# Kernel tuning notes

Measured on AMD Instinct MI355X. Metric: run time of the kernel, lower is better.

## Reference

```python
import jax, jax.numpy as jnp
import numpy as np


def setup_inputs() -> dict:
    key = jax.random.key(0)
    k1, k2 = jax.random.split(key)
    pred = jax.random.normal(k1, (4, 4096, 3), dtype=jnp.float32)
    gt = jax.random.normal(k2, (4, 4096, 3), dtype=jnp.float32)
    return {"pred": pred, "gt": gt}


def reference(pred, gt):
    # Chamfer distance with L1 (Manhattan) point-to-point distance.
    # pred: [B, N, 3], gt: [B, M, 3]
    # d[b, n, m] = sum_c |pred[b,n,c] - gt[b,m,c]|
    d = jnp.abs(pred[:, :, None, :] - gt[:, None, :, :]).sum(-1)  # [B, N, M]
    cham_x = d.min(axis=2).mean(axis=1)  # nearest gt for each pred point, [B]
    cham_y = d.min(axis=1).mean(axis=1)  # nearest pred for each gt point, [B]
    # point_reduction='mean' per direction, batch_reduction='mean' (pytorch3d default)
    return jnp.mean(cham_x + cham_y)
```

## Files before the change

### kernel.cpp

```cpp
#include <hip/hip_runtime.h>
#include <cfloat>


constexpr int TPB = 256;
constexpr int PTS = 4;
constexpr int NC  = TPB * PTS;
constexpr int MC  = 256;

__global__ __launch_bounds__(TPB) void chamfer_partial_kernel(
    const float* __restrict__ pred, const float* __restrict__ gt,
    unsigned* __restrict__ wsmin, int B, int N, int M) {
    const int dir = blockIdx.z;
    const int b   = blockIdx.y;
    const float* q = dir ? gt   : pred;
    const float* t = dir ? pred : gt;
    const int Nq   = dir ? M : N;
    const int Nt   = dir ? N : M;
    const int nchunks = Nq / NC;
    const int nc = blockIdx.x % nchunks;
    const int mc = blockIdx.x / nchunks;

    __shared__ float4 lds4[MC];

    const float* tbase = t + ((size_t)b * Nt + (size_t)mc * MC) * 3;
    for (int i = threadIdx.x; i < MC * 3; i += TPB) {
        ((float*)&lds4[i / 3])[i % 3] = tbase[i];
    }
    __syncthreads();

    const float* qb = q + (size_t)b * Nq * 3;
    float px[PTS], py[PTS], pz[PTS], mn[PTS];
    int n[PTS];
#pragma unroll
    for (int i = 0; i < PTS; ++i) {
        n[i] = nc * NC + threadIdx.x + i * TPB;
        px[i] = qb[n[i] * 3 + 0];
        py[i] = qb[n[i] * 3 + 1];
        pz[i] = qb[n[i] * 3 + 2];
        mn[i] = FLT_MAX;
    }

#pragma unroll 4
    for (int j = 0; j < MC; j += 2) {
        float4 g0 = lds4[j];
        float4 g1 = lds4[j + 1];
#pragma unroll
        for (int i = 0; i < PTS; ++i) {
            float d0 = fabsf(px[i] - g0.x) + fabsf(py[i] - g0.y) + fabsf(pz[i] - g0.z);
            float d1 = fabsf(px[i] - g1.x) + fabsf(py[i] - g1.y) + fabsf(pz[i] - g1.z);
            mn[i] = fminf(mn[i], fminf(d0, d1));
        }
    }

    unsigned* outp = wsmin + ((size_t)dir * B + b) * N;
#pragma unroll
    for (int i = 0; i < PTS; ++i)
        atomicMin(&outp[n[i]], __float_as_uint(mn[i]));
}

__global__ __launch_bounds__(256) void chamfer_reduce_kernel(
    const unsigned* __restrict__ wsmin, float* __restrict__ out, float inv) {
    const int qidx = blockIdx.x * 256 + threadIdx.x;
    float v = __uint_as_float(wsmin[qidx]) * inv;

    for (int off = 32; off > 0; off >>= 1) v += __shfl_down(v, off, 64);
    __shared__ float red[4];
    const int lane = threadIdx.x & 63, w = threadIdx.x >> 6;
    if (lane == 0) red[w] = v;
    __syncthreads();
    if (threadIdx.x == 0)
        atomicAdd(out, red[0] + red[1] + red[2] + red[3]);
}

extern "C" void kernel_launch(void* const* d_in, const int* in_sizes, int n_in,
                              void* d_out, int out_size, void* d_ws, size_t ws_size,
                              hipStream_t stream) {
    const float* pred = (const float*)d_in[0];
    const float* gt   = (const float*)d_in[1];
    float* out = (float*)d_out;

    const int B = 4;
    const int N = in_sizes[0] / (B * 3);
    const int M = in_sizes[1] / (B * 3);

    unsigned* wsmin = (unsigned*)d_ws;
    const int nmc = M / MC;
    const int Q = 2 * B * N;

    hipMemsetAsync(out, 0, sizeof(float), stream);
    hipMemsetAsync(wsmin, 0xFF, (size_t)Q * sizeof(unsigned), stream);

    dim3 grid((N / NC) * nmc, B, 2);
    chamfer_partial_kernel<<<grid, TPB, 0, stream>>>(pred, gt, wsmin, B, N, M);

    chamfer_reduce_kernel<<<Q / 256, 256, 0, stream>>>(
        wsmin, out, 1.0f / (float)(B * N));
}
```

Measured before the change: 79.15 us.

## Fuse final reduction into partial kernel via last-block counter and SoA LDS

Merges the reduce kernel into the distance kernel: each block increments a global counter after its atomicMin writes, and the last block to arrive sums all per-point minima and writes the output directly. This removes one kernel launch and one memset. It also changes the shared-memory tile from float4-per-point to a structure-of-arrays layout, so each float4 read covers four target points per coordinate and the inner loop processes four points per step. The counter starts at 0xFFFFFFFF from the memset, which is why the last-block test compares against nblocks-2. The cost is a serial final sum over all minima inside a single block.

```diff
diff --git a/kernel.cpp b/kernel.cpp
--- a/kernel.cpp
+++ b/kernel.cpp
@@ -7,9 +7,11 @@
 constexpr int NC  = TPB * PTS;
 constexpr int MC  = 256;
 
-__global__ __launch_bounds__(TPB) void chamfer_partial_kernel(
+__global__ __launch_bounds__(TPB) void chamfer_fused_kernel(
     const float* __restrict__ pred, const float* __restrict__ gt,
-    unsigned* __restrict__ wsmin, int B, int N, int M) {
+    unsigned* __restrict__ wsmin, unsigned* __restrict__ counter,
+    float* __restrict__ out,
+    int B, int N, int M, int nblocks, float inv) {
     const int dir = blockIdx.z;
     const int b   = blockIdx.y;
     const float* q = dir ? gt   : pred;
@@ -20,11 +22,13 @@
     const int nc = blockIdx.x % nchunks;
     const int mc = blockIdx.x / nchunks;
 
-    __shared__ float4 lds4[MC];
+    __shared__ __align__(16) float lds[3 * MC];
+    __shared__ float red[4];
+    __shared__ int lastFlag;
 
     const float* tbase = t + ((size_t)b * Nt + (size_t)mc * MC) * 3;
     for (int i = threadIdx.x; i < MC * 3; i += TPB) {
-        ((float*)&lds4[i / 3])[i % 3] = tbase[i];
+        lds[(i % 3) * MC + i / 3] = tbase[i];
     }
     __syncthreads();
 
@@ -40,15 +44,19 @@
         mn[i] = FLT_MAX;
     }
 
-#pragma unroll 4
-    for (int j = 0; j < MC; j += 2) {
-        float4 g0 = lds4[j];
-        float4 g1 = lds4[j + 1];
+#pragma unroll 2
+    for (int j = 0; j < MC; j += 4) {
+        float4 gx = *(const float4*)&lds[j];
+        float4 gy = *(const float4*)&lds[MC + j];
+        float4 gz = *(const float4*)&lds[2 * MC + j];
 #pragma unroll
         for (int i = 0; i < PTS; ++i) {
-            float d0 = fabsf(px[i] - g0.x) + fabsf(py[i] - g0.y) + fabsf(pz[i] - g0.z);
-            float d1 = fabsf(px[i] - g1.x) + fabsf(py[i] - g1.y) + fabsf(pz[i] - g1.z);
+            float d0 = fabsf(px[i] - gx.x) + fabsf(py[i] - gy.x) + fabsf(pz[i] - gz.x);
+            float d1 = fabsf(px[i] - gx.y) + fabsf(py[i] - gy.y) + fabsf(pz[i] - gz.y);
+            float d2 = fabsf(px[i] - gx.z) + fabsf(py[i] - gy.z) + fabsf(pz[i] - gz.z);
+            float d3 = fabsf(px[i] - gx.w) + fabsf(py[i] - gy.w) + fabsf(pz[i] - gz.w);
             mn[i] = fminf(mn[i], fminf(d0, d1));
+            mn[i] = fminf(mn[i], fminf(d2, d3));
         }
     }
 
@@ -56,20 +64,33 @@
 #pragma unroll
     for (int i = 0; i < PTS; ++i)
         atomicMin(&outp[n[i]], __float_as_uint(mn[i]));
-}
 
-__global__ __launch_bounds__(256) void chamfer_reduce_kernel(
-    const unsigned* __restrict__ wsmin, float* __restrict__ out, float inv) {
-    const int qidx = blockIdx.x * 256 + threadIdx.x;
-    float v = __uint_as_float(wsmin[qidx]) * inv;
+    __threadfence();
+    if (threadIdx.x == 0) {
+        unsigned old = __hip_atomic_fetch_add(counter, 1u, __ATOMIC_ACQ_REL,
+                                              __HIP_MEMORY_SCOPE_AGENT);
+        lastFlag = (old == (unsigned)(nblocks - 2));
+    }
+    __syncthreads();
+    if (!lastFlag) return;
+    __threadfence();
+
+    const unsigned long long* w2 = (const unsigned long long*)wsmin;
+    const int total2 = B * N;
+    float v = 0.0f;
+    for (int i = threadIdx.x; i < total2; i += TPB) {
+        unsigned long long u = __hip_atomic_load(&w2[i], __ATOMIC_RELAXED,
+                                                 __HIP_MEMORY_SCOPE_AGENT);
+        v += __uint_as_float((unsigned)u) + __uint_as_float((unsigned)(u >> 32));
+    }
+    v *= inv;
 
     for (int off = 32; off > 0; off >>= 1) v += __shfl_down(v, off, 64);
-    __shared__ float red[4];
     const int lane = threadIdx.x & 63, w = threadIdx.x >> 6;
     if (lane == 0) red[w] = v;
     __syncthreads();
     if (threadIdx.x == 0)
-        atomicAdd(out, red[0] + red[1] + red[2] + red[3]);
+        *out = red[0] + red[1] + red[2] + red[3];
 }
 
 extern "C" void kernel_launch(void* const* d_in, const int* in_sizes, int n_in,
@@ -83,16 +104,15 @@
     const int N = in_sizes[0] / (B * 3);
     const int M = in_sizes[1] / (B * 3);
 
-    unsigned* wsmin = (unsigned*)d_ws;
-    const int nmc = M / MC;
+    unsigned* wsmin   = (unsigned*)d_ws;
     const int Q = 2 * B * N;
+    unsigned* counter = wsmin + Q;
 
-    hipMemsetAsync(out, 0, sizeof(float), stream);
-    hipMemsetAsync(wsmin, 0xFF, (size_t)Q * sizeof(unsigned), stream);
+    hipMemsetAsync(d_ws, 0xFF, (size_t)(Q + 16) * sizeof(unsigned), stream);
 
-    dim3 grid((N / NC) * nmc, B, 2);
-    chamfer_partial_kernel<<<grid, TPB, 0, stream>>>(pred, gt, wsmin, B, N, M);
-
-    chamfer_reduce_kernel<<<Q / 256, 256, 0, stream>>>(
-        wsmin, out, 1.0f / (float)(B * N));
+    dim3 grid((N / NC) * (M / MC), B, 2);
+    const int nblocks = grid.x * grid.y * grid.z;
+    chamfer_fused_kernel<<<grid, TPB, 0, stream>>>(
+        pred, gt, wsmin, counter, out, B, N, M, nblocks,
+        1.0f / (float)(B * N));
 }
```

Result: slower. 121.8 us (+53.9%).
